# Kernel tuning notes

Hardware: AMD Instinct MI355X
Metric: run time of the kernel (lower is better)

## Reference

```python
import jax, jax.numpy as jnp
import numpy as np

B, IN_CH, OUT_CH, H, W = 8, 64, 128, 128, 128
K = 3          # i2h kernel
L = 5          # number of flow fields
FLOW_HID = 32  # hidden channels of flow generator
NEG_SLOPE = 0.2


def _conv(x, w, b, pad):
    y = jax.lax.conv_general_dilated(x, w, (1, 1), [(pad, pad), (pad, pad)],
                                     dimension_numbers=('NCHW', 'OIHW', 'NCHW'))
    return y + b[None, :, None, None]


def _leaky(x):
    return jnp.where(x >= 0, x, NEG_SLOPE * x)


def _bilinear(img, px, py):
    # img [B,C,H,W]; px,py [B,H,W] pixel coords. Bilinear, zero padding,
    # align_corners=True semantics (normalization by W-1 cancels out -> pixel coords).
    Bs, C, Hs, Ws = img.shape
    x0 = jnp.floor(px); y0 = jnp.floor(py)
    wx = px - x0; wy = py - y0
    bidx = jnp.arange(Bs)[:, None, None]
    def g(xi, yi):
        valid = (xi >= 0) & (xi <= Ws - 1) & (yi >= 0) & (yi <= Hs - 1)
        xc = jnp.clip(xi, 0, Ws - 1).astype(jnp.int32)
        yc = jnp.clip(yi, 0, Hs - 1).astype(jnp.int32)
        v = img[bidx, :, yc, xc]  # [B,H,W,C]
        return jnp.where(valid[..., None], v, jnp.zeros((), img.dtype))
    out = ((1 - wy)[..., None] * ((1 - wx)[..., None] * g(x0, y0) + wx[..., None] * g(x0 + 1, y0))
           + wy[..., None] * ((1 - wx)[..., None] * g(x0, y0 + 1) + wx[..., None] * g(x0 + 1, y0 + 1)))
    return out.transpose(0, 3, 1, 2)  # [B,C,H,W]


def _trajgru_step(x, h, i2h_w, i2h_b, i2f_w, i2f_b, h2f_w, h2f_b, flow_w, flow_b, ret_w, ret_b):
    Bs, F, Hs, Ws = h.shape
    # flow generator
    f1 = _leaky(_conv(x, i2f_w, i2f_b, 2) + _conv(h, h2f_w, h2f_b, 2))
    flows = _conv(f1, flow_w, flow_b, 2).reshape(Bs, L, 2, Hs, Ws)
    # warp hidden state: wrap(h, -flow) => sample at grid - flow
    xx = jnp.arange(Ws, dtype=x.dtype)[None, :]
    yy = jnp.arange(Hs, dtype=x.dtype)[:, None]
    px = xx[None, None] - flows[:, :, 0]  # [B,L,H,W]
    py = yy[None, None] - flows[:, :, 1]
    warped = jax.vmap(_bilinear, in_axes=(None, 1, 1), out_axes=1)(h, px, py)  # [B,L,F,H,W]
    h2h = _conv(warped.reshape(Bs, L * F, Hs, Ws), ret_w, ret_b, 0)  # [B,3F,H,W]
    i2h = _conv(x, i2h_w, i2h_b, K // 2)                             # [B,3F,H,W]
    r = jax.nn.sigmoid(i2h[:, :F] + h2h[:, :F])
    u = jax.nn.sigmoid(i2h[:, F:2 * F] + h2h[:, F:2 * F])
    new_mem = _leaky(i2h[:, 2 * F:] + r * h2h[:, 2 * F:])
    return u * h + (1 - u) * new_mem


def setup_inputs() -> dict:
    key = jax.random.key(0)
    ks = jax.random.split(key, 16)
    d = {}
    d['x'] = jax.random.normal(ks[0], (B, IN_CH, H, W), jnp.float32)
    d['h_prev1'] = jnp.zeros((B, OUT_CH, H, W), jnp.float32)
    d['h_prev2'] = jnp.zeros((B, OUT_CH, H, W), jnp.float32)
    def mk(k, shape):
        return jax.random.normal(k, shape, jnp.float32) * 0.05
    i = 1
    for s, cin in (('1', IN_CH), ('2', OUT_CH)):
        d['i2h_w' + s] = mk(ks[i], (3 * OUT_CH, cin, K, K)); i += 1
        d['i2h_b' + s] = jnp.zeros((3 * OUT_CH,), jnp.float32)
        d['i2f_w' + s] = mk(ks[i], (FLOW_HID, cin, 5, 5)); i += 1
        d['i2f_b' + s] = jnp.zeros((FLOW_HID,), jnp.float32)
        d['h2f_w' + s] = mk(ks[i], (FLOW_HID, OUT_CH, 5, 5)); i += 1
        d['h2f_b' + s] = jnp.zeros((FLOW_HID,), jnp.float32)
        d['flow_w' + s] = mk(ks[i], (2 * L, FLOW_HID, 5, 5)); i += 1
        d['flow_b' + s] = jnp.zeros((2 * L,), jnp.float32)
        d['ret_w' + s] = mk(ks[i], (3 * OUT_CH, L * OUT_CH, 1, 1)); i += 1
        d['ret_b' + s] = jnp.zeros((3 * OUT_CH,), jnp.float32)
    return d


def reference(x, h_prev1, h_prev2,
              i2h_w1, i2h_b1, i2f_w1, i2f_b1, h2f_w1, h2f_b1, flow_w1, flow_b1, ret_w1, ret_b1,
              i2h_w2, i2h_b2, i2f_w2, i2f_b2, h2f_w2, h2f_b2, flow_w2, flow_b2, ret_w2, ret_b2):
    h1 = _trajgru_step(x, h_prev1, i2h_w1, i2h_b1, i2f_w1, i2f_b1, h2f_w1, h2f_b1,
                       flow_w1, flow_b1, ret_w1, ret_b1)
    h2 = _trajgru_step(h1, h_prev2, i2h_w2, i2h_b2, i2f_w2, i2f_b2, h2f_w2, h2f_b2,
                       flow_w2, flow_b2, ret_w2, ret_b2)
    return h2
```

## Files before the change

kernel.cpp:

```cpp
#include <hip/hip_runtime.h>
#include <hip/hip_bf16.h>
#include <cstdint>
#include <cstddef>

#define HH 128
#define WW 128
#define HW 16384
#define NEGS 0.2f

typedef __attribute__((ext_vector_type(8))) short short8;
typedef __attribute__((ext_vector_type(4))) short s16x4;
typedef __attribute__((ext_vector_type(4))) float f32x4;

__device__ __forceinline__ float leakyf(float v) { return v >= 0.f ? v : NEGS * v; }
__device__ __forceinline__ float sigmf_(float v) { return 1.f / (1.f + __expf(-v)); }
__device__ __forceinline__ float bf2f(short s) {
  union { float f; unsigned u; } x;
  x.u = ((unsigned)(unsigned short)s) << 16;
  return x.f;
}
__device__ __forceinline__ short f2bf(float v) {
  __hip_bfloat16 h = __float2bfloat16(v);
  return *(short*)&h;
}

__global__ __launch_bounds__(256) void k_pack(const float* __restrict__ src,
                                              __hip_bfloat16* __restrict__ dst,
                                              int OC, int CINs, int T, int kbase,
                                              int KK) {
  int i = blockIdx.x * 256 + threadIdx.x;
  if (i >= OC * CINs * T) return;
  int t = i % T;
  int c = (i / T) % CINs;
  int oc = i / (T * CINs);
  dst[(size_t)oc * KK + kbase + t * CINs + c] = __float2bfloat16(src[i]);
}

template <int CH>
__global__ __launch_bounds__(256) void k_cast_nhwc(const float* __restrict__ in,
                                                   __hip_bfloat16* __restrict__ out) {
  __shared__ float t[32][33];
  int bx = blockIdx.x;
  int cx = blockIdx.y;
  int bz = blockIdx.z;
  int b = bz >> 7, y = bz & 127;
  int tx = threadIdx.x & 31, tg = threadIdx.x >> 5;
#pragma unroll
  for (int i = 0; i < 4; ++i) {
    int c = cx * 32 + tg * 4 + i;
    t[tg * 4 + i][tx] = in[(((size_t)b * CH + c) * 128 + y) * 128 + bx * 32 + tx];
  }
  __syncthreads();
#pragma unroll
  for (int i = 0; i < 4; ++i) {
    int x = bx * 32 + tg * 4 + i;
    size_t pix = ((size_t)b * 128 + y) * 128 + x;
    out[pix * CH + cx * 32 + tx] = __float2bfloat16(t[tx][tg * 4 + i]);
  }
}

__global__ __launch_bounds__(256) void k_tonchw(const float* __restrict__ in,
                                                float* __restrict__ out) {
  __shared__ float t[32][33];
  int bx = blockIdx.x;
  int cx = blockIdx.y;
  int bz = blockIdx.z;
  int b = bz >> 7, y = bz & 127;
  int tx = threadIdx.x & 31, tg = threadIdx.x >> 5;
#pragma unroll
  for (int i = 0; i < 4; ++i) {
    int x = bx * 32 + tg * 4 + i;
    t[tg * 4 + i][tx] = in[(((size_t)b * 128 + y) * 128 + x) * 128 + cx * 32 + tx];
  }
  __syncthreads();
#pragma unroll
  for (int i = 0; i < 4; ++i) {
    int c = cx * 32 + tg * 4 + i;
    out[(((size_t)b * 128 + c) * 128 + y) * 128 + bx * 32 + tx] = t[tx][tg * 4 + i];
  }
}

template <int CS, int NFR, int KK>
__device__ __forceinline__ void fc_do(const short* __restrict__ src,
                                      const short* __restrict__ wrow,
                                      int wk, int c0, int tap,
                                      int b, int y, int xb0, int l15, int lk,
                                      f32x4 (&acc)[4][NFR]) {
  int dy = tap / 5 - 2, dx = tap % 5 - 2;
  int yy = y + dy;
  bool yok = (unsigned)yy < 128u;
  short8 bf[NFR];
#pragma unroll
  for (int fn = 0; fn < NFR; ++fn)
    bf[fn] = *(const short8*)&wrow[(size_t)(fn * 16) * KK + wk];
  const short8 z = {0, 0, 0, 0, 0, 0, 0, 0};
  const short* rbase = src + ((size_t)b * 16384 + (size_t)(yok ? yy : 0) * 128) * CS + c0 + lk;
  short8 af[4];
#pragma unroll
  for (int fm = 0; fm < 4; ++fm) {
    int xx = xb0 + fm * 16 + l15 + dx;
    bool ok = yok && ((unsigned)xx < 128u);
    short8 v = *(const short8*)(rbase + (size_t)(ok ? xx : 0) * CS);
    af[fm] = ok ? v : z;
  }
#pragma unroll
  for (int fm = 0; fm < 4; ++fm)
#pragma unroll
    for (int fn = 0; fn < NFR; ++fn)
      acc[fm][fn] = __builtin_amdgcn_mfma_f32_16x16x32_bf16(
          af[fm], bf[fn], acc[fm][fn], 0, 0, 0);
}

template <int CIN1, int CIN2, int NFR, int NSY>
__global__ __launch_bounds__(256) void k_fconv(
    const short* __restrict__ in1, const short* __restrict__ in2,
    const short* __restrict__ wb, float* __restrict__ acco) {
  constexpr int KK = 25 * (CIN1 + CIN2);
  constexpr int C1 = CIN1 / 32;
  constexpr int C2 = (CIN2 > 0) ? CIN2 / 32 : 1;
  constexpr int NS = 4 * NSY;
  int tid = threadIdx.x, lane = tid & 63, w = tid >> 6;
  int l15 = lane & 15, lk = (lane >> 4) * 8;
  int subset = blockIdx.y * 4 + w;
  int p0 = blockIdx.x * 64;
  int b = p0 >> 14;
  int y = (p0 >> 7) & 127;
  int xb0 = p0 & 127;

  f32x4 acc[4][NFR];
#pragma unroll
  for (int i = 0; i < 4; ++i)
#pragma unroll
    for (int j = 0; j < NFR; ++j) {
      acc[i][j][0] = 0.f; acc[i][j][1] = 0.f;
      acc[i][j][2] = 0.f; acc[i][j][3] = 0.f;
    }

  const short* wrow = wb + (size_t)l15 * KK + lk;

  for (int ci = subset; ci < 25 * C1; ci += NS) {
    int tap = ci / C1;
    int c0 = (ci % C1) * 32;
    fc_do<CIN1, NFR, KK>(in1, wrow, tap * CIN1 + c0, c0, tap, b, y, xb0, l15,
                         lk, acc);
  }
  if constexpr (CIN2 > 0) {
    for (int ci = subset; ci < 25 * C2; ci += NS) {
      int tap = ci / C2;
      int c0 = (ci % C2) * 32;
      fc_do<CIN2, NFR, KK>(in2, wrow, 25 * CIN1 + tap * CIN2 + c0, c0, tap, b,
                           y, xb0, l15, lk, acc);
    }
  }

#pragma unroll
  for (int fn = 0; fn < NFR; ++fn) {
    int ocx = fn * 16 + l15;
#pragma unroll
    for (int fm = 0; fm < 4; ++fm)
#pragma unroll
      for (int j = 0; j < 4; ++j) {
        int m = fm * 16 + (lane >> 4) * 4 + j;
        atomicAdd(&acco[(size_t)(p0 + m) * (NFR * 16) + ocx], acc[fm][fn][j]);
      }
  }
}

template <int CW, bool LEAKY, bool OUTBF16>
__global__ __launch_bounds__(256) void k_ffin(const float* __restrict__ acc,
                                              const float* __restrict__ b1,
                                              const float* __restrict__ b2,
                                              void* __restrict__ outp,
                                              int nvalid) {
  size_t gid = (size_t)blockIdx.x * 256 + threadIdx.x;
  int c4 = (int)((gid * 4) & (CW - 1));
  f32x4 v = *(const f32x4*)(acc + gid * 4);
  if (OUTBF16) {
    s16x4 o;
#pragma unroll
    for (int j = 0; j < 4; ++j) {
      int c = c4 + j;
      float bv = b1[c] + (b2 ? b2[c] : 0.f);
      float r = v[j] + bv;
      if (LEAKY) r = leakyf(r);
      o[j] = f2bf(r);
    }
    *(s16x4*)((short*)outp + gid * 4) = o;
  } else {
    f32x4 o;
#pragma unroll
    for (int j = 0; j < 4; ++j) {
      int c = c4 + j;
      float r = 0.f;
      if (c < nvalid) {
        float bv = b1[c] + (b2 ? b2[c] : 0.f);
        r = v[j] + bv;
        if (LEAKY) r = leakyf(r);
      }
      o[j] = r;
    }
    *(f32x4*)((float*)outp + gid * 4) = o;
  }
}

template <int CS, int NFR, int KK>
__device__ __forceinline__ void mc_seg(const short* __restrict__ src,
                                       const short* __restrict__ wrow,
                                       int kbase, int dy, int dx,
                                       const int* py_r, const int* px_m,
                                       int lk, f32x4 (&acc)[4][NFR]) {
  const short* aptr[4];
  bool av[4];
#pragma unroll
  for (int fm = 0; fm < 4; ++fm) {
    int yy = (py_r[fm] & 127) + dy;
    int bb = py_r[fm] >> 7;
    int xx = px_m[fm] + dx;
    bool ok = ((unsigned)yy < 128u) && ((unsigned)xx < 128u);
    av[fm] = ok;
    int ycl = ok ? yy : 0;
    int xcl = ok ? xx : 0;
    size_t pix = ((size_t)(bb << 7) + ycl) * 128 + xcl;
    aptr[fm] = src + pix * CS + lk;
  }
  const short8 z = {0, 0, 0, 0, 0, 0, 0, 0};
#pragma unroll
  for (int c0 = 0; c0 < CS; c0 += 32) {
    short8 bf[NFR];
#pragma unroll
    for (int fn = 0; fn < NFR; ++fn)
      bf[fn] = *(const short8*)&wrow[(size_t)fn * 16 * KK + kbase + c0];
    short8 af[4];
#pragma unroll
    for (int fm = 0; fm < 4; ++fm) {
      short8 v = *(const short8*)(aptr[fm] + c0);
      af[fm] = av[fm] ? v : z;
    }
#pragma unroll
    for (int fm = 0; fm < 4; ++fm)
#pragma unroll
      for (int fn = 0; fn < NFR; ++fn)
        acc[fm][fn] = __builtin_amdgcn_mfma_f32_16x16x32_bf16(
            af[fm], bf[fn], acc[fm][fn], 0, 0, 0);
  }
}

template <int CIN1, int RAD, int BN, int MODE>
__global__ __launch_bounds__(256) void k_mconv(
    const short* __restrict__ in1, const short* __restrict__ wb,
    const float* __restrict__ bias1, void* __restrict__ outp,
    void* __restrict__ outp2, int nout, int ostride) {
  constexpr int KD = 2 * RAD + 1;
  constexpr int T = KD * KD;
  constexpr int KK = T * CIN1;
  constexpr int WN = 2;
  constexpr int NFR = BN / 32;

  int tid = threadIdx.x, lane = tid & 63, wid = tid >> 6;
  int wm = wid / WN, wn = wid % WN;
  int l15 = lane & 15, lk = (lane >> 4) * 8;
  int r0 = blockIdx.x;
  int ocb = blockIdx.y * BN + wn * (NFR * 16);

  f32x4 acc[4][NFR];
#pragma unroll
  for (int i = 0; i < 4; ++i)
#pragma unroll
    for (int j = 0; j < NFR; ++j) {
      acc[i][j][0] = 0.f; acc[i][j][1] = 0.f;
      acc[i][j][2] = 0.f; acc[i][j][3] = 0.f;
    }

  int py_r[4], px_m[4];
#pragma unroll
  for (int fm = 0; fm < 4; ++fm) {
    int m = wm * 64 + fm * 16 + l15;
    py_r[fm] = r0 + (m >> 7);
    px_m[fm] = m & 127;
  }

  const short* wrow = wb + (size_t)(ocb + l15) * KK + lk;

#pragma unroll 1
  for (int s = 0; s < T; ++s) {
    int dy = s / KD - RAD, dx = s % KD - RAD;
    mc_seg<CIN1, NFR, KK>(in1, wrow, s * CIN1, dy, dx, py_r, px_m, lk, acc);
  }

#pragma unroll
  for (int fn = 0; fn < NFR; ++fn) {
    int ocx = ocb + fn * 16 + l15;
    float bv = bias1[ocx];
#pragma unroll
    for (int fm = 0; fm < 4; ++fm) {
#pragma unroll
      for (int j = 0; j < 4; ++j) {
        int m = wm * 64 + fm * 16 + (lane >> 4) * 4 + j;
        int row = r0 + (m >> 7);
        size_t pix = (size_t)row * 128 + (m & 127);
        float v = acc[fm][fn][j] + bv;
        if constexpr (MODE == 0)
          ((float*)outp)[pix * ostride + ocx] = v;
        else {
          if (ocx < 256)
            ((float*)outp)[pix * 384 + ocx] += v;
          else
            ((float*)outp2)[pix * 128 + (ocx - 256)] = v;
        }
      }
    }
  }
}

__global__ __launch_bounds__(256) void k_warp5(
    const __hip_bfloat16* __restrict__ h_t, const float* __restrict__ flows,
    __hip_bfloat16* __restrict__ wout) {
  int t = threadIdx.x;
  int c = t & 127;
  size_t n = (size_t)blockIdx.x * 2 + (t >> 7);
  int b = (int)(n >> 14);
  int p = (int)(n & 16383);
  int y = p >> 7, x = p & 127;
  const __hip_bfloat16* base = h_t + (size_t)b * HW * 128;
#pragma unroll 1
  for (int l = 0; l < 5; ++l) {
    float fx = flows[n * 16 + 2 * l];
    float fy = flows[n * 16 + 2 * l + 1];
    float px = (float)x - fx;
    float py = (float)y - fy;
    float x0f = floorf(px), y0f = floorf(py);
    float wx = px - x0f, wy = py - y0f;
    int x0 = (int)x0f, y0i = (int)y0f;
    float v00 = 0.f, v10 = 0.f, v01 = 0.f, v11 = 0.f;
    if ((unsigned)x0 <= 127u && (unsigned)y0i <= 127u)
      v00 = __bfloat162float(base[((size_t)y0i * WW + x0) * 128 + c]);
    if ((unsigned)(x0 + 1) <= 127u && (unsigned)y0i <= 127u)
      v10 = __bfloat162float(base[((size_t)y0i * WW + (x0 + 1)) * 128 + c]);
    if ((unsigned)x0 <= 127u && (unsigned)(y0i + 1) <= 127u)
      v01 = __bfloat162float(base[((size_t)(y0i + 1) * WW + x0) * 128 + c]);
    if ((unsigned)(x0 + 1) <= 127u && (unsigned)(y0i + 1) <= 127u)
      v11 = __bfloat162float(base[((size_t)(y0i + 1) * WW + (x0 + 1)) * 128 + c]);
    float v = (1.f - wy) * ((1.f - wx) * v00 + wx * v10) +
              wy * ((1.f - wx) * v01 + wx * v11);
    wout[n * 640 + l * 128 + c] = __float2bfloat16(v);
  }
}

template <bool FINAL>
__global__ __launch_bounds__(256) void k_gates2(
    const float* __restrict__ i2h, const float* __restrict__ h2h,
    const __hip_bfloat16* __restrict__ hpt, void* __restrict__ outp) {
  int tid = threadIdx.x;
  size_t n = (size_t)blockIdx.x * 8 + (tid >> 5);
  int c4 = (tid & 31) * 4;
  const float* irow = i2h + n * 384;
  f32x4 a0 = *(const f32x4*)(irow + c4);
  f32x4 a1 = *(const f32x4*)(irow + 128 + c4);
  f32x4 a2 = *(const f32x4*)(irow + 256 + c4);
  f32x4 b2 = *(const f32x4*)(h2h + n * 128 + c4);
  s16x4 hv = *(const s16x4*)((const short*)hpt + n * 128 + c4);
  if (FINAL) {
    f32x4 o;
#pragma unroll
    for (int j = 0; j < 4; ++j) {
      float r = sigmf_(a0[j]), u = sigmf_(a1[j]);
      float nm = leakyf(fmaf(r, b2[j], a2[j]));
      o[j] = u * bf2f(hv[j]) + (1.f - u) * nm;
    }
    *(f32x4*)((float*)outp + n * 128 + c4) = o;
  } else {
    s16x4 o;
#pragma unroll
    for (int j = 0; j < 4; ++j) {
      float r = sigmf_(a0[j]), u = sigmf_(a1[j]);
      float nm = leakyf(fmaf(r, b2[j], a2[j]));
      o[j] = f2bf(u * bf2f(hv[j]) + (1.f - u) * nm);
    }
    *(s16x4*)((short*)outp + n * 128 + c4) = o;
  }
}

extern "C" void kernel_launch(void* const* d_in, const int* in_sizes, int n_in,
                              void* d_out, int out_size, void* d_ws, size_t ws_size,
                              hipStream_t stream) {
  const float* x       = (const float*)d_in[0];
  const float* hp1     = (const float*)d_in[1];
  const float* hp2     = (const float*)d_in[2];
  const float* i2h_w1  = (const float*)d_in[3];
  const float* i2h_b1  = (const float*)d_in[4];
  const float* i2f_w1  = (const float*)d_in[5];
  const float* i2f_b1  = (const float*)d_in[6];
  const float* h2f_w1  = (const float*)d_in[7];
  const float* h2f_b1  = (const float*)d_in[8];
  const float* flow_w1 = (const float*)d_in[9];
  const float* flow_b1 = (const float*)d_in[10];
  const float* ret_w1  = (const float*)d_in[11];
  const float* ret_b1  = (const float*)d_in[12];
  const float* i2h_w2  = (const float*)d_in[13];
  const float* i2h_b2  = (const float*)d_in[14];
  const float* i2f_w2  = (const float*)d_in[15];
  const float* i2f_b2  = (const float*)d_in[16];
  const float* h2f_w2  = (const float*)d_in[17];
  const float* h2f_b2  = (const float*)d_in[18];
  const float* flow_w2 = (const float*)d_in[19];
  const float* flow_b2 = (const float*)d_in[20];
  const float* ret_w2  = (const float*)d_in[21];
  const float* ret_b2  = (const float*)d_in[22];
  float* out = (float*)d_out;

  const size_t nWb3_1 = (size_t)384 * 576;
  const size_t nWb3_2 = (size_t)384 * 1152;
  const size_t nWbf1  = (size_t)32 * 4800;
  const size_t nWbf2  = (size_t)32 * 6400;
  const size_t nWfl   = (size_t)16 * 800;
  const size_t nWret  = (size_t)384 * 640;
  const size_t wtot = nWb3_1 + nWb3_2 + nWbf1 + nWbf2 + 2 * nWfl + 2 * nWret;

  int NBC = 8;
  while (NBC > 1 && wtot * 2 + (size_t)4096 * NBC * HW > ws_size)
    NBC >>= 1;
  const int npixc = NBC * HW;

  __hip_bfloat16* wbase = (__hip_bfloat16*)d_ws;
  __hip_bfloat16* Wb3_1 = wbase;
  __hip_bfloat16* Wb3_2 = Wb3_1 + nWb3_1;
  __hip_bfloat16* Wbf1  = Wb3_2 + nWb3_2;
  __hip_bfloat16* Wbf2  = Wbf1 + nWbf1;
  __hip_bfloat16* Wfl1  = Wbf2 + nWbf2;
  __hip_bfloat16* Wfl2  = Wfl1 + nWfl;
  __hip_bfloat16* Wret1 = Wfl2 + nWfl;
  __hip_bfloat16* Wret2 = Wret1 + nWret;

  char* abase = (char*)(Wret2 + nWret);
  float* i2hbuf = (float*)abase;
  float* h2hbuf = i2hbuf + (size_t)npixc * 384;
  __hip_bfloat16* warpb5 = (__hip_bfloat16*)(h2hbuf + (size_t)npixc * 128);
  __hip_bfloat16* h_t = warpb5 + (size_t)npixc * 640;
  __hip_bfloat16* xb  = h_t + (size_t)npixc * 128;
  __hip_bfloat16* f1b = xb + (size_t)npixc * 128;
  float* flowsb = (float*)(f1b + (size_t)npixc * 32);
  float* facc = flowsb + (size_t)npixc * 16;
  float* go = (float*)warpb5;

  dim3 blk(256);
  auto packs = [&](const float* src, __hip_bfloat16* dst, int OC, int CINs,
                   int T, int kbase, int KK) {
    int n = OC * CINs * T;
    k_pack<<<dim3((n + 255) / 256), blk, 0, stream>>>(src, dst, OC, CINs, T,
                                                      kbase, KK);
  };
  packs(i2h_w1, Wb3_1, 384, 64, 9, 0, 576);
  packs(i2h_w2, Wb3_2, 384, 128, 9, 0, 1152);
  packs(i2f_w1, Wbf1, 32, 64, 25, 0, 4800);
  packs(h2f_w1, Wbf1, 32, 128, 25, 1600, 4800);
  packs(i2f_w2, Wbf2, 32, 128, 25, 0, 6400);
  packs(h2f_w2, Wbf2, 32, 128, 25, 3200, 6400);
  packs(flow_w1, Wfl1, 10, 32, 25, 0, 800);
  packs(flow_w2, Wfl2, 10, 32, 25, 0, 800);
  packs(ret_w1, Wret1, 384, 640, 1, 0, 640);
  packs(ret_w2, Wret2, 384, 640, 1, 0, 640);

  for (int b0 = 0; b0 < 8; b0 += NBC) {
    const float* xc   = x + (size_t)b0 * 64 * HW;
    const float* hp1c = hp1 + (size_t)b0 * 128 * HW;
    const float* hp2c = hp2 + (size_t)b0 * 128 * HW;

    k_cast_nhwc<128><<<dim3(4, 4, NBC * 128), blk, 0, stream>>>(hp1c, h_t);
    k_cast_nhwc<64><<<dim3(4, 2, NBC * 128), blk, 0, stream>>>(xc, xb);
    hipMemsetAsync(facc, 0, (size_t)npixc * 32 * 4, stream);
    k_fconv<64, 128, 2, 2><<<dim3(npixc / 64, 2), blk, 0, stream>>>(
        (const short*)xb, (const short*)h_t, (const short*)Wbf1, facc);
    k_ffin<32, true, true><<<dim3(npixc * 32 / 1024), blk, 0, stream>>>(
        facc, i2f_b1, h2f_b1, f1b, 32);
    hipMemsetAsync(facc, 0, (size_t)npixc * 16 * 4, stream);
    k_fconv<32, 0, 1, 1><<<dim3(npixc / 64, 1), blk, 0, stream>>>(
        (const short*)f1b, nullptr, (const short*)Wfl1, facc);
    k_ffin<16, false, false><<<dim3(npixc * 16 / 1024), blk, 0, stream>>>(
        facc, flow_b1, nullptr, flowsb, 10);
    k_mconv<64, 1, 128, 0><<<dim3(NBC * 128, 3), blk, 0, stream>>>(
        (const short*)xb, (const short*)Wb3_1, i2h_b1, i2hbuf, nullptr, 384, 384);
    k_warp5<<<dim3(npixc / 2), blk, 0, stream>>>(h_t, flowsb, warpb5);
    k_mconv<640, 0, 128, 2><<<dim3(NBC * 128, 3), blk, 0, stream>>>(
        (const short*)warpb5, (const short*)Wret1, ret_b1, i2hbuf, h2hbuf, 384, 384);
    k_gates2<false><<<dim3(npixc / 8), blk, 0, stream>>>(i2hbuf, h2hbuf, h_t, xb);

    k_cast_nhwc<128><<<dim3(4, 4, NBC * 128), blk, 0, stream>>>(hp2c, h_t);
    hipMemsetAsync(facc, 0, (size_t)npixc * 32 * 4, stream);
    k_fconv<128, 128, 2, 2><<<dim3(npixc / 64, 2), blk, 0, stream>>>(
        (const short*)xb, (const short*)h_t, (const short*)Wbf2, facc);
    k_ffin<32, true, true><<<dim3(npixc * 32 / 1024), blk, 0, stream>>>(
        facc, i2f_b2, h2f_b2, f1b, 32);
    hipMemsetAsync(facc, 0, (size_t)npixc * 16 * 4, stream);
    k_fconv<32, 0, 1, 1><<<dim3(npixc / 64, 1), blk, 0, stream>>>(
        (const short*)f1b, nullptr, (const short*)Wfl2, facc);
    k_ffin<16, false, false><<<dim3(npixc * 16 / 1024), blk, 0, stream>>>(
        facc, flow_b2, nullptr, flowsb, 10);
    k_mconv<128, 1, 128, 0><<<dim3(NBC * 128, 3), blk, 0, stream>>>(
        (const short*)xb, (const short*)Wb3_2, i2h_b2, i2hbuf, nullptr, 384, 384);
    k_warp5<<<dim3(npixc / 2), blk, 0, stream>>>(h_t, flowsb, warpb5);
    k_mconv<640, 0, 128, 2><<<dim3(NBC * 128, 3), blk, 0, stream>>>(
        (const short*)warpb5, (const short*)Wret2, ret_b2, i2hbuf, h2hbuf, 384, 384);
    k_gates2<true><<<dim3(npixc / 8), blk, 0, stream>>>(i2hbuf, h2hbuf, h_t, go);
    k_tonchw<<<dim3(4, 4, NBC * 128), blk, 0, stream>>>(go, out + (size_t)b0 * 128 * HW);
  }
}
```

Before: 3.039 ms.

## Pre-swizzle weights and warped activations into MFMA fragment layout for mconv

Weights for the i2h and ret convolutions are packed into a per-16-channel, per-32-k fragment-major layout, so each lane loads its MFMA B fragment with one contiguous 16-byte read. The warp kernel now writes its output in the same fragment-major layout, which gives the 1x1 ret convolution fully coalesced A loads. The mconv kernel is restructured into a single flat k-chunk loop with simpler address math, and its output tile is halved (BN 128 to 64) to double the grid. The intent is to cut strided global loads and address overhead in the main GEMM-like convolutions. In exchange, the warp kernel's stores become scattered and each activation tile is reloaded by twice as many blocks.

```diff
diff --git a/kernel.cpp b/kernel.cpp
--- a/kernel.cpp
+++ b/kernel.cpp
@@ -34,6 +34,21 @@
   int c = (i / T) % CINs;
   int oc = i / (T * CINs);
   dst[(size_t)oc * KK + kbase + t * CINs + c] = __float2bfloat16(src[i]);
+}
+
+__global__ __launch_bounds__(256) void k_packs(const float* __restrict__ src,
+                                               __hip_bfloat16* __restrict__ dst,
+                                               int OC, int CINs, int T) {
+  int KK = T * CINs;
+  int idx = blockIdx.x * 256 + threadIdx.x;
+  if (idx >= OC * KK) return;
+  int oc = idx / KK, k = idx % KK;
+  int t = k / CINs, c = k % CINs;
+  float v = src[((size_t)oc * CINs + c) * T + t];
+  int octile = oc >> 4, o16 = oc & 15;
+  int kc = k >> 5, kg = (k >> 3) & 3, i = k & 7;
+  size_t d = (((size_t)octile * (KK >> 5) + kc) * 64 + kg * 16 + o16) * 8 + i;
+  dst[d] = __float2bfloat16(v);
 }
 
 template <int CH>
@@ -203,39 +218,67 @@
   }
 }
 
-template <int CS, int NFR, int KK>
-__device__ __forceinline__ void mc_seg(const short* __restrict__ src,
-                                       const short* __restrict__ wrow,
-                                       int kbase, int dy, int dx,
-                                       const int* py_r, const int* px_m,
-                                       int lk, f32x4 (&acc)[4][NFR]) {
-  const short* aptr[4];
-  bool av[4];
-#pragma unroll
-  for (int fm = 0; fm < 4; ++fm) {
-    int yy = (py_r[fm] & 127) + dy;
-    int bb = py_r[fm] >> 7;
-    int xx = px_m[fm] + dx;
-    bool ok = ((unsigned)yy < 128u) && ((unsigned)xx < 128u);
-    av[fm] = ok;
-    int ycl = ok ? yy : 0;
-    int xcl = ok ? xx : 0;
-    size_t pix = ((size_t)(bb << 7) + ycl) * 128 + xcl;
-    aptr[fm] = src + pix * CS + lk;
-  }
+template <int CIN1, int RAD, int MODE, bool ASWZ>
+__global__ __launch_bounds__(256) void k_mconv(
+    const short* __restrict__ in1, const short* __restrict__ wb,
+    const float* __restrict__ bias1, void* __restrict__ outp,
+    void* __restrict__ outp2) {
+  constexpr int KD = 2 * RAD + 1;
+  constexpr int T = KD * KD;
+  constexpr int KK = T * CIN1;
+  constexpr int NCH = KK / 32;
+  constexpr int CPT = CIN1 / 32;
+  constexpr int NFR = 2;
+
+  int tid = threadIdx.x, lane = tid & 63, wid = tid >> 6;
+  int wm = wid >> 1, wn = wid & 1;
+  int l15 = lane & 15, lk4 = lane >> 4;
+  int r0 = blockIdx.x;
+  int ocb = blockIdx.y * 64 + wn * 32;
+  int octb = ocb >> 4;
+  int b = r0 >> 7, y = r0 & 127;
+
+  f32x4 acc[4][NFR];
+#pragma unroll
+  for (int i = 0; i < 4; ++i)
+#pragma unroll
+    for (int j = 0; j < NFR; ++j) {
+      acc[i][j][0] = 0.f; acc[i][j][1] = 0.f;
+      acc[i][j][2] = 0.f; acc[i][j][3] = 0.f;
+    }
+
   const short8 z = {0, 0, 0, 0, 0, 0, 0, 0};
-#pragma unroll
-  for (int c0 = 0; c0 < CS; c0 += 32) {
+
+#pragma unroll 2
+  for (int kc = 0; kc < NCH; ++kc) {
+    short8 af[4];
+    if constexpr (ASWZ) {
+#pragma unroll
+      for (int fm = 0; fm < 4; ++fm) {
+        size_t pixblock = (size_t)r0 * 8 + wm * 4 + fm;
+        af[fm] = *(const short8*)&in1[((pixblock * NCH + kc) * 64 + lane) * 8];
+      }
+    } else {
+      int s = kc / CPT;
+      int c0 = (kc % CPT) * 32;
+      int dy = s / KD - RAD, dx = s % KD - RAD;
+      int yy = y + dy;
+      bool yok = (unsigned)yy < 128u;
+      const short* rbase =
+          in1 + ((size_t)b * 16384 + (size_t)(yok ? yy : 0) * 128) * CIN1 + c0 +
+          lk4 * 8;
+#pragma unroll
+      for (int fm = 0; fm < 4; ++fm) {
+        int xx = wm * 64 + fm * 16 + l15 + dx;
+        bool ok = yok && ((unsigned)xx < 128u);
+        short8 v = *(const short8*)(rbase + (size_t)(ok ? xx : 0) * CIN1);
+        af[fm] = ok ? v : z;
+      }
+    }
     short8 bf[NFR];
 #pragma unroll
     for (int fn = 0; fn < NFR; ++fn)
-      bf[fn] = *(const short8*)&wrow[(size_t)fn * 16 * KK + kbase + c0];
-    short8 af[4];
-#pragma unroll
-    for (int fm = 0; fm < 4; ++fm) {
-      short8 v = *(const short8*)(aptr[fm] + c0);
-      af[fm] = av[fm] ? v : z;
-    }
+      bf[fn] = *(const short8*)&wb[(((size_t)(octb + fn) * NCH + kc) * 64 + lane) * 8];
 #pragma unroll
     for (int fm = 0; fm < 4; ++fm)
 #pragma unroll
@@ -243,49 +286,6 @@
         acc[fm][fn] = __builtin_amdgcn_mfma_f32_16x16x32_bf16(
             af[fm], bf[fn], acc[fm][fn], 0, 0, 0);
   }
-}
-
-template <int CIN1, int RAD, int BN, int MODE>
-__global__ __launch_bounds__(256) void k_mconv(
-    const short* __restrict__ in1, const short* __restrict__ wb,
-    const float* __restrict__ bias1, void* __restrict__ outp,
-    void* __restrict__ outp2, int nout, int ostride) {
-  constexpr int KD = 2 * RAD + 1;
-  constexpr int T = KD * KD;
-  constexpr int KK = T * CIN1;
-  constexpr int WN = 2;
-  constexpr int NFR = BN / 32;
-
-  int tid = threadIdx.x, lane = tid & 63, wid = tid >> 6;
-  int wm = wid / WN, wn = wid % WN;
-  int l15 = lane & 15, lk = (lane >> 4) * 8;
-  int r0 = blockIdx.x;
-  int ocb = blockIdx.y * BN + wn * (NFR * 16);
-
-  f32x4 acc[4][NFR];
-#pragma unroll
-  for (int i = 0; i < 4; ++i)
-#pragma unroll
-    for (int j = 0; j < NFR; ++j) {
-      acc[i][j][0] = 0.f; acc[i][j][1] = 0.f;
-      acc[i][j][2] = 0.f; acc[i][j][3] = 0.f;
-    }
-
-  int py_r[4], px_m[4];
-#pragma unroll
-  for (int fm = 0; fm < 4; ++fm) {
-    int m = wm * 64 + fm * 16 + l15;
-    py_r[fm] = r0 + (m >> 7);
-    px_m[fm] = m & 127;
-  }
-
-  const short* wrow = wb + (size_t)(ocb + l15) * KK + lk;
-
-#pragma unroll 1
-  for (int s = 0; s < T; ++s) {
-    int dy = s / KD - RAD, dx = s % KD - RAD;
-    mc_seg<CIN1, NFR, KK>(in1, wrow, s * CIN1, dy, dx, py_r, px_m, lk, acc);
-  }
 
 #pragma unroll
   for (int fn = 0; fn < NFR; ++fn) {
@@ -295,12 +295,11 @@
     for (int fm = 0; fm < 4; ++fm) {
 #pragma unroll
       for (int j = 0; j < 4; ++j) {
-        int m = wm * 64 + fm * 16 + (lane >> 4) * 4 + j;
-        int row = r0 + (m >> 7);
-        size_t pix = (size_t)row * 128 + (m & 127);
+        int m = wm * 64 + fm * 16 + lk4 * 4 + j;
+        size_t pix = (size_t)r0 * 128 + m;
         float v = acc[fm][fn][j] + bv;
         if constexpr (MODE == 0)
-          ((float*)outp)[pix * ostride + ocx] = v;
+          ((float*)outp)[pix * 384 + ocx] = v;
         else {
           if (ocx < 256)
             ((float*)outp)[pix * 384 + ocx] += v;
@@ -321,6 +320,8 @@
   int b = (int)(n >> 14);
   int p = (int)(n & 16383);
   int y = p >> 7, x = p & 127;
+  size_t pixblock = n >> 4;
+  int p16 = (int)(n & 15);
   const __hip_bfloat16* base = h_t + (size_t)b * HW * 128;
 #pragma unroll 1
   for (int l = 0; l < 5; ++l) {
@@ -342,7 +343,10 @@
       v11 = __bfloat162float(base[((size_t)(y0i + 1) * WW + (x0 + 1)) * 128 + c]);
     float v = (1.f - wy) * ((1.f - wx) * v00 + wx * v10) +
               wy * ((1.f - wx) * v01 + wx * v11);
-    wout[n * 640 + l * 128 + c] = __float2bfloat16(v);
+    int cc = l * 128 + c;
+    int kc = cc >> 5, kg = (cc >> 3) & 3, i = cc & 7;
+    wout[((pixblock * 20 + kc) * 64 + kg * 16 + p16) * 8 + i] =
+        __float2bfloat16(v);
   }
 }
 
@@ -443,22 +447,27 @@
   float* go = (float*)warpb5;
 
   dim3 blk(256);
-  auto packs = [&](const float* src, __hip_bfloat16* dst, int OC, int CINs,
+  auto packl = [&](const float* src, __hip_bfloat16* dst, int OC, int CINs,
                    int T, int kbase, int KK) {
     int n = OC * CINs * T;
     k_pack<<<dim3((n + 255) / 256), blk, 0, stream>>>(src, dst, OC, CINs, T,
                                                       kbase, KK);
   };
-  packs(i2h_w1, Wb3_1, 384, 64, 9, 0, 576);
-  packs(i2h_w2, Wb3_2, 384, 128, 9, 0, 1152);
-  packs(i2f_w1, Wbf1, 32, 64, 25, 0, 4800);
-  packs(h2f_w1, Wbf1, 32, 128, 25, 1600, 4800);
-  packs(i2f_w2, Wbf2, 32, 128, 25, 0, 6400);
-  packs(h2f_w2, Wbf2, 32, 128, 25, 3200, 6400);
-  packs(flow_w1, Wfl1, 10, 32, 25, 0, 800);
-  packs(flow_w2, Wfl2, 10, 32, 25, 0, 800);
-  packs(ret_w1, Wret1, 384, 640, 1, 0, 640);
-  packs(ret_w2, Wret2, 384, 640, 1, 0, 640);
+  auto packsw = [&](const float* src, __hip_bfloat16* dst, int OC, int CINs,
+                    int T) {
+    int n = OC * CINs * T;
+    k_packs<<<dim3((n + 255) / 256), blk, 0, stream>>>(src, dst, OC, CINs, T);
+  };
+  packsw(i2h_w1, Wb3_1, 384, 64, 9);
+  packsw(i2h_w2, Wb3_2, 384, 128, 9);
+  packsw(ret_w1, Wret1, 384, 640, 1);
+  packsw(ret_w2, Wret2, 384, 640, 1);
+  packl(i2f_w1, Wbf1, 32, 64, 25, 0, 4800);
+  packl(h2f_w1, Wbf1, 32, 128, 25, 1600, 4800);
+  packl(i2f_w2, Wbf2, 32, 128, 25, 0, 6400);
+  packl(h2f_w2, Wbf2, 32, 128, 25, 3200, 6400);
+  packl(flow_w1, Wfl1, 10, 32, 25, 0, 800);
+  packl(flow_w2, Wfl2, 10, 32, 25, 0, 800);
 
   for (int b0 = 0; b0 < 8; b0 += NBC) {
     const float* xc   = x + (size_t)b0 * 64 * HW;
@@ -477,11 +486,11 @@
         (const short*)f1b, nullptr, (const short*)Wfl1, facc);
     k_ffin<16, false, false><<<dim3(npixc * 16 / 1024), blk, 0, stream>>>(
         facc, flow_b1, nullptr, flowsb, 10);
-    k_mconv<64, 1, 128, 0><<<dim3(NBC * 128, 3), blk, 0, stream>>>(
-        (const short*)xb, (const short*)Wb3_1, i2h_b1, i2hbuf, nullptr, 384, 384);
+    k_mconv<64, 1, 0, false><<<dim3(NBC * 128, 6), blk, 0, stream>>>(
+        (const short*)xb, (const short*)Wb3_1, i2h_b1, i2hbuf, nullptr);
     k_warp5<<<dim3(npixc / 2), blk, 0, stream>>>(h_t, flowsb, warpb5);
-    k_mconv<640, 0, 128, 2><<<dim3(NBC * 128, 3), blk, 0, stream>>>(
-        (const short*)warpb5, (const short*)Wret1, ret_b1, i2hbuf, h2hbuf, 384, 384);
+    k_mconv<640, 0, 2, true><<<dim3(NBC * 128, 6), blk, 0, stream>>>(
+        (const short*)warpb5, (const short*)Wret1, ret_b1, i2hbuf, h2hbuf);
     k_gates2<false><<<dim3(npixc / 8), blk, 0, stream>>>(i2hbuf, h2hbuf, h_t, xb);
 
     k_cast_nhwc<128><<<dim3(4, 4, NBC * 128), blk, 0, stream>>>(hp2c, h_t);
@@ -495,11 +504,11 @@
         (const short*)f1b, nullptr, (const short*)Wfl2, facc);
     k_ffin<16, false, false><<<dim3(npixc * 16 / 1024), blk, 0, stream>>>(
         facc, flow_b2, nullptr, flowsb, 10);
-    k_mconv<128, 1, 128, 0><<<dim3(NBC * 128, 3), blk, 0, stream>>>(
-        (const short*)xb, (const short*)Wb3_2, i2h_b2, i2hbuf, nullptr, 384, 384);
+    k_mconv<128, 1, 0, false><<<dim3(NBC * 128, 6), blk, 0, stream>>>(
+        (const short*)xb, (const short*)Wb3_2, i2h_b2, i2hbuf, nullptr);
     k_warp5<<<dim3(npixc / 2), blk, 0, stream>>>(h_t, flowsb, warpb5);
-    k_mconv<640, 0, 128, 2><<<dim3(NBC * 128, 3), blk, 0, stream>>>(
-        (const short*)warpb5, (const short*)Wret2, ret_b2, i2hbuf, h2hbuf, 384, 384);
+    k_mconv<640, 0, 2, true><<<dim3(NBC * 128, 6), blk, 0, stream>>>(
+        (const short*)warpb5, (const short*)Wret2, ret_b2, i2hbuf, h2hbuf);
     k_gates2<true><<<dim3(npixc / 8), blk, 0, stream>>>(i2hbuf, h2hbuf, h_t, go);
     k_tonchw<<<dim3(4, 4, NBC * 128), blk, 0, stream>>>(go, out + (size_t)b0 * 128 * HW);
   }
```

After: 2.715 ms. 1.12x faster.
